# Optimization experiments

Measured on AMD Instinct MI355X. Metric: run time of the kernel, lower is better.

The kernel has to match this reference:

```python
import jax, jax.numpy as jnp
import numpy as np

DIM, DEPTH, HEADS, DIM_HEAD, MLP = 768, 6, 12, 64, 3072
INNER = HEADS * DIM_HEAD
B, N = 8, 1024
SCALE = DIM_HEAD ** -0.5
EPS = 1e-5


def _ln(x, g, b):
    m = jnp.mean(x, -1, keepdims=True)
    v = jnp.mean(jnp.square(x - m), -1, keepdims=True)
    return (x - m) * jax.lax.rsqrt(v + EPS) * g + b


def _ternary(w):
    # BitNet-style ternary quant with straight-through estimator
    s = jnp.mean(jnp.abs(w)) + 1e-8
    wq = jnp.clip(jnp.round(w / s), -1.0, 1.0) * s
    return w + jax.lax.stop_gradient(wq - w)


def setup_inputs() -> dict:
    key = jax.random.key(0)
    ks = jax.random.split(key, 8)
    d = {
        'x': jax.random.normal(ks[0], (B, N, DIM), jnp.float32),
        'ln1_g': jnp.ones((DEPTH, DIM), jnp.float32),
        'ln1_b': jnp.zeros((DEPTH, DIM), jnp.float32),
        'Wqkv': jax.random.normal(ks[1], (DEPTH, 3 * INNER, DIM), jnp.float32) * 0.02,
        'ln2_g': jnp.ones((DEPTH, INNER), jnp.float32),
        'ln2_b': jnp.zeros((DEPTH, INNER), jnp.float32),
        'Wo': jax.random.normal(ks[2], (DEPTH, DIM, INNER), jnp.float32) * 0.02,
        'bo': jnp.zeros((DEPTH, DIM), jnp.float32),
        'ffln1_g': jnp.ones((DEPTH, DIM), jnp.float32),
        'ffln1_b': jnp.zeros((DEPTH, DIM), jnp.float32),
        'W1': jax.random.normal(ks[3], (DEPTH, MLP, DIM), jnp.float32) * 0.02,
        'b1': jnp.zeros((DEPTH, MLP), jnp.float32),
        'ffln2_g': jnp.ones((DEPTH, MLP), jnp.float32),
        'ffln2_b': jnp.zeros((DEPTH, MLP), jnp.float32),
        'W2': jax.random.normal(ks[4], (DEPTH, DIM, MLP), jnp.float32) * 0.02,
        'b2': jnp.zeros((DEPTH, DIM), jnp.float32),
    }
    return d


def _forward(x, ln1_g, ln1_b, Wqkv, ln2_g, ln2_b, Wo, bo,
             ffln1_g, ffln1_b, W1, b1, ffln2_g, ffln2_b, W2, b2):
    depth = Wqkv.shape[0]
    # layers 0..depth-2 ternary, last layer plain linear
    flag = jnp.concatenate([jnp.ones((depth - 1,), x.dtype), jnp.zeros((1,), x.dtype)])

    def block(h, p):
        (g1, b1n, wqkv, g2, b2n, wo, bo_, fg1, fb1, w1, bb1, fg2, fb2, w2, bb2, f) = p

        def mt(w):
            return f * _ternary(w) + (1.0 - f) * w

        y = _ln(h, g1, b1n)
        qkv = jnp.einsum('bnd,ed->bne', y, mt(wqkv))  # [B,N,3*INNER]
        q, k, v = jnp.split(qkv, 3, axis=-1)
        def heads(t):
            return t.reshape(B, N, HEADS, DIM_HEAD).transpose(0, 2, 1, 3)
        q, k, v = heads(q), heads(k), heads(v)
        attn = jax.nn.softmax(jnp.einsum('bhnd,bhmd->bhnm', q, k) * SCALE, axis=-1)
        o = jnp.einsum('bhnm,bhmd->bhnd', attn, v)
        o = o.transpose(0, 2, 1, 3).reshape(B, N, INNER)
        o = _ln(o, g2, b2n)
        o = jnp.einsum('bne,de->bnd', o, mt(wo)) + bo_
        h = h + o
        y = _ln(h, fg1, fb1)
        y = jnp.einsum('bnd,md->bnm', y, mt(w1)) + bb1
        y = jax.nn.gelu(y, approximate=False)
        y = _ln(y, fg2, fb2)
        y = jnp.einsum('bnm,dm->bnd', y, mt(w2)) + bb2
        return h + y, None

    xs = (ln1_g, ln1_b, Wqkv, ln2_g, ln2_b, Wo, bo,
          ffln1_g, ffln1_b, W1, b1, ffln2_g, ffln2_b, W2, b2, flag)
    out, _ = jax.lax.scan(block, x, xs)
    return out


def reference(x, ln1_g, ln1_b, Wqkv, ln2_g, ln2_b, Wo, bo,
              ffln1_g, ffln1_b, W1, b1, ffln2_g, ffln2_b, W2, b2):
    return _forward(x, ln1_g, ln1_b, Wqkv, ln2_g, ln2_b, Wo, bo,
                    ffln1_g, ffln1_b, W1, b1, ffln2_g, ffln2_b, W2, b2)
```

## Files before the change

### kernel.cpp

```cpp
#include <hip/hip_runtime.h>
#include <hip/hip_bf16.h>
#include <math.h>

typedef __bf16 bf16_t;
typedef __bf16 bf16x4 __attribute__((ext_vector_type(4)));
typedef __bf16 bf16x8 __attribute__((ext_vector_type(8)));
typedef float  f32x4  __attribute__((ext_vector_type(4)));

#define TOKENS 8192
#define DIMV   768
#define INNERV 768
#define QKVW   2304
#define MLPW   3072
#define NSEQ   1024
#define NB     8
#define NH     12
#define DH     64

enum { EP_STORE = 0, EP_BIAS_RES = 1, EP_BIAS_GELU = 2 };

__device__ __forceinline__ void gload_lds16(const bf16_t* g, bf16_t* l)
{
  __builtin_amdgcn_global_load_lds((const __attribute__((address_space(1))) void*)g,
                                   (__attribute__((address_space(3))) void*)l,
                                   16, 0, 0);
}

__global__ __launch_bounds__(256)
void gemm_nt(const bf16_t* __restrict__ A, const bf16_t* __restrict__ B,
             const int K, const int N, const int mode,
             const float* __restrict__ sacc_p, const float sinvn, const float sbias,
             const float* __restrict__ bias,
             float* __restrict__ resid,
             bf16_t* __restrict__ outb,
             float* __restrict__ fout)
{
  __shared__ __align__(16) bf16_t lsA[2][128 * 32];
  __shared__ __align__(16) bf16_t lsB[2][128 * 32];
  const int tid  = threadIdx.x;
  const int lane = tid & 63;
  const int wave = tid >> 6;
  const int wm = wave >> 1, wn = wave & 1;
  const int bm = blockIdx.x, bn = blockIdx.y;

  const int srow = wave * 32 + (lane >> 2);
  const int fsw  = (srow >> 1) & 3;
  const int scol = ((lane & 3) ^ fsw) * 8;
  const bf16_t* gA = A + (size_t)(bm * 128 + srow) * K + scol;
  const bf16_t* gB = B + (size_t)(bn * 128 + srow) * K + scol;
  const int l0 = srow * 32 + (lane & 3) * 8;
  const int l1 = (srow + 16) * 32 + (lane & 3) * 8;

  f32x4 acc[4][4];
#pragma unroll
  for (int i = 0; i < 4; i++)
#pragma unroll
    for (int j = 0; j < 4; j++) acc[i][j] = (f32x4){0.f, 0.f, 0.f, 0.f};

  const int fr   = ((lane & 15) >> 1) & 3;
  const int rsl  = ((lane >> 4) ^ fr) * 8;
  const int arow = (wm * 64 + (lane & 15)) * 32 + rsl;
  const int brow = (wn * 64 + (lane & 15)) * 32 + rsl;

  auto stage = [&](int b, int kb) {
    gload_lds16(gA + kb,                  &lsA[b][l0]);
    gload_lds16(gA + (size_t)16 * K + kb, &lsA[b][l1]);
    gload_lds16(gB + kb,                  &lsB[b][l0]);
    gload_lds16(gB + (size_t)16 * K + kb, &lsB[b][l1]);
  };
  auto compute = [&](int b) {
    bf16x8 af[4], bfv[4];
#pragma unroll
    for (int i = 0; i < 4; i++) af[i]  = *(const bf16x8*)&lsA[b][arow + i * 16 * 32];
#pragma unroll
    for (int j = 0; j < 4; j++) bfv[j] = *(const bf16x8*)&lsB[b][brow + j * 16 * 32];
#pragma unroll
    for (int i = 0; i < 4; i++)
#pragma unroll
      for (int j = 0; j < 4; j++)
        acc[i][j] = __builtin_amdgcn_mfma_f32_16x16x32_bf16(af[i], bfv[j], acc[i][j], 0, 0, 0);
  };

  const int NT = K / 32;
  stage(0, 0);
  stage(1, 32);
  int cur = 0;
  for (int t = 0; t < NT - 1; ++t) {
    asm volatile("s_waitcnt vmcnt(4)" ::: "memory");
    __builtin_amdgcn_s_barrier();
    __builtin_amdgcn_sched_barrier(0);
    compute(cur);
    asm volatile("s_waitcnt lgkmcnt(0)" ::: "memory");
    __builtin_amdgcn_s_barrier();
    __builtin_amdgcn_sched_barrier(0);
    if (t + 2 < NT) stage(cur, (t + 2) * 32);
    cur ^= 1;
  }
  asm volatile("s_waitcnt vmcnt(0)" ::: "memory");
  __builtin_amdgcn_s_barrier();
  __builtin_amdgcn_sched_barrier(0);
  compute(cur);

  const float s = (*sacc_p) * sinvn + sbias;
  const int r0 = bm * 128 + wm * 64 + (lane >> 4) * 4;
  const int c0 = bn * 128 + wn * 64 + (lane & 15);
#pragma unroll
  for (int i = 0; i < 4; i++) {
#pragma unroll
    for (int j = 0; j < 4; j++) {
      const int col = c0 + j * 16;
#pragma unroll
      for (int r = 0; r < 4; r++) {
        const int row = r0 + i * 16 + r;
        const float v = acc[i][j][r] * s;
        const size_t idx = (size_t)row * N + col;
        if (mode == EP_STORE) {
          outb[idx] = (bf16_t)v;
        } else if (mode == EP_BIAS_RES) {
          const float add = v + bias[col];
          if (fout) fout[idx] = resid[idx] + add;
          else      resid[idx] += add;
        } else {
          const float t = v + bias[col];
          outb[idx] = (bf16_t)(0.5f * t * (1.0f + erff(t * 0.70710678118654752f)));
        }
      }
    }
  }
}

template <typename TIN>
__global__ __launch_bounds__(256)
void ln_kern(const TIN* __restrict__ x, const float* __restrict__ g,
             const float* __restrict__ b, bf16_t* __restrict__ y, const int W)
{
  const int row = blockIdx.x;
  const int tid = threadIdx.x;
  const TIN* xr = x + (size_t)row * W;
  float s = 0.f, s2 = 0.f;
  if constexpr (sizeof(TIN) == 4) {
    const f32x4* xv = (const f32x4*)xr;
    for (int i = tid; i < W / 4; i += 256) {
      f32x4 v = xv[i];
#pragma unroll
      for (int e = 0; e < 4; e++) { s += v[e]; s2 += v[e] * v[e]; }
    }
  } else {
    const bf16x8* xv = (const bf16x8*)xr;
    for (int i = tid; i < W / 8; i += 256) {
      bf16x8 v = xv[i];
#pragma unroll
      for (int e = 0; e < 8; e++) { const float f = (float)v[e]; s += f; s2 += f * f; }
    }
  }
#pragma unroll
  for (int off = 32; off > 0; off >>= 1) {
    s  += __shfl_xor(s,  off, 64);
    s2 += __shfl_xor(s2, off, 64);
  }
  __shared__ float red[8];
  if ((tid & 63) == 0) { red[(tid >> 6) * 2] = s; red[(tid >> 6) * 2 + 1] = s2; }
  __syncthreads();
  const float ts  = red[0] + red[2] + red[4] + red[6];
  const float ts2 = red[1] + red[3] + red[5] + red[7];
  const float invW = 1.0f / (float)W;
  const float mean = ts * invW;
  const float var  = fmaxf(ts2 * invW - mean * mean, 0.f);
  const float rs   = rsqrtf(var + 1e-5f);
  bf16_t* yr = y + (size_t)row * W;
  const f32x4* gv = (const f32x4*)g;
  const f32x4* bv = (const f32x4*)b;
  if constexpr (sizeof(TIN) == 4) {
    const f32x4* xv = (const f32x4*)xr;
    bf16x4* yv = (bf16x4*)yr;
    for (int i = tid; i < W / 4; i += 256) {
      f32x4 v = xv[i], gg = gv[i], bb = bv[i];
      bf16x4 o;
#pragma unroll
      for (int e = 0; e < 4; e++) o[e] = (bf16_t)((v[e] - mean) * rs * gg[e] + bb[e]);
      yv[i] = o;
    }
  } else {
    const bf16x8* xv = (const bf16x8*)xr;
    bf16x8* yv = (bf16x8*)yr;
    for (int i = tid; i < W / 8; i += 256) {
      bf16x8 v = xv[i];
      f32x4 g0 = gv[2 * i], g1 = gv[2 * i + 1];
      f32x4 b0 = bv[2 * i], b1 = bv[2 * i + 1];
      bf16x8 o;
#pragma unroll
      for (int e = 0; e < 4; e++) o[e]     = (bf16_t)(((float)v[e]     - mean) * rs * g0[e] + b0[e]);
#pragma unroll
      for (int e = 0; e < 4; e++) o[e + 4] = (bf16_t)(((float)v[e + 4] - mean) * rs * g1[e] + b1[e]);
      yv[i] = o;
    }
  }
}

__global__ __launch_bounds__(256)
void attn_mfma(const bf16_t* __restrict__ qkv, bf16_t* __restrict__ o)
{
  __shared__ __align__(16) bf16_t Ks[64][72];
  __shared__ __align__(16) bf16_t Vt[64][72];
  __shared__ __align__(16) bf16_t Pw[4][16][72];
  const float SCL = 0.125f * 1.44269504088896f;
  const int tid  = threadIdx.x;
  const int lane = tid & 63;
  const int wave = tid >> 6;
  const int quad = lane >> 4;
  const int l15  = lane & 15;
  const int qb = blockIdx.x, hh = blockIdx.y, bb = blockIdx.z;
  const size_t tokbase = (size_t)bb * NSEQ;

  const int qrow = qb * 64 + wave * 16 + l15;
  bf16x8 qf[2];
  {
    const bf16_t* qp = qkv + (tokbase + qrow) * QKVW + hh * DH;
    qf[0] = *(const bf16x8*)(qp + quad * 8);
    qf[1] = *(const bf16x8*)(qp + 32 + quad * 8);
  }

  f32x4 Ot[4];
#pragma unroll
  for (int i = 0; i < 4; i++) Ot[i] = (f32x4){0.f, 0.f, 0.f, 0.f};
  float m2[4], lp[4];
#pragma unroll
  for (int r = 0; r < 4; r++) { m2[r] = -1e30f; lp[r] = 0.f; }

  const int skv = tid & 63;
  const int sd  = (tid >> 6) * 16;

  bf16x8 k0, k1, v0, v1;
  {
    const bf16_t* kp = qkv + (tokbase + skv) * QKVW + INNERV + hh * DH + sd;
    k0 = *(const bf16x8*)kp;
    k1 = *(const bf16x8*)(kp + 8);
    v0 = *(const bf16x8*)(kp + INNERV);
    v1 = *(const bf16x8*)(kp + INNERV + 8);
  }

  for (int kt = 0; kt < NSEQ / 64; ++kt) {
    __syncthreads();
    *(bf16x8*)&Ks[skv][sd]     = k0;
    *(bf16x8*)&Ks[skv][sd + 8] = k1;
#pragma unroll
    for (int e = 0; e < 8; e++) { Vt[sd + e][skv] = v0[e]; Vt[sd + 8 + e][skv] = v1[e]; }
    __syncthreads();

    bf16x8 nk0 = k0, nk1 = k1, nv0 = v0, nv1 = v1;
    if (kt + 1 < NSEQ / 64) {
      const bf16_t* kp = qkv + (tokbase + (kt + 1) * 64 + skv) * QKVW + INNERV + hh * DH + sd;
      nk0 = *(const bf16x8*)kp;
      nk1 = *(const bf16x8*)(kp + 8);
      nv0 = *(const bf16x8*)(kp + INNERV);
      nv1 = *(const bf16x8*)(kp + INNERV + 8);
    }

    f32x4 st[4];
    __builtin_amdgcn_s_setprio(1);
#pragma unroll
    for (int nt = 0; nt < 4; nt++) {
      bf16x8 b0 = *(const bf16x8*)&Ks[nt * 16 + l15][quad * 8];
      bf16x8 b1 = *(const bf16x8*)&Ks[nt * 16 + l15][32 + quad * 8];
      f32x4 c = (f32x4){0.f, 0.f, 0.f, 0.f};
      c = __builtin_amdgcn_mfma_f32_16x16x32_bf16(qf[0], b0, c, 0, 0, 0);
      c = __builtin_amdgcn_mfma_f32_16x16x32_bf16(qf[1], b1, c, 0, 0, 0);
      st[nt] = c;
    }
    __builtin_amdgcn_s_setprio(0);

    float rmax2[4];
#pragma unroll
    for (int r = 0; r < 4; r++) {
      float v = fmaxf(fmaxf(st[0][r], st[1][r]), fmaxf(st[2][r], st[3][r]));
      v = fmaxf(v, __shfl_xor(v, 1, 64));
      v = fmaxf(v, __shfl_xor(v, 2, 64));
      v = fmaxf(v, __shfl_xor(v, 4, 64));
      v = fmaxf(v, __shfl_xor(v, 8, 64));
      rmax2[r] = v * SCL;
    }
    const bool ok = (rmax2[0] <= m2[0] + 8.f) && (rmax2[1] <= m2[1] + 8.f) &&
                    (rmax2[2] <= m2[2] + 8.f) && (rmax2[3] <= m2[3] + 8.f);
    if (!__all(ok)) {
#pragma unroll
      for (int r = 0; r < 4; r++) {
        const float mnew = fmaxf(m2[r], rmax2[r]);
        const float alpha = exp2f(m2[r] - mnew);
        m2[r] = mnew;
        lp[r] *= alpha;
#pragma unroll
        for (int dt = 0; dt < 4; dt++) Ot[dt][r] *= alpha;
      }
    }
#pragma unroll
    for (int nt = 0; nt < 4; nt++) {
#pragma unroll
      for (int r = 0; r < 4; r++) {
        const float p = exp2f(fmaf(st[nt][r], SCL, -m2[r]));
        lp[r] += p;
        Pw[wave][quad * 4 + r][nt * 16 + l15] = (bf16_t)p;
      }
    }

    asm volatile("s_waitcnt lgkmcnt(0)" ::: "memory");
    __builtin_amdgcn_sched_barrier(0);

    __builtin_amdgcn_s_setprio(1);
#pragma unroll
    for (int kk = 0; kk < 2; kk++) {
      bf16x8 pa = *(const bf16x8*)&Pw[wave][l15][kk * 32 + quad * 8];
#pragma unroll
      for (int dt = 0; dt < 4; dt++) {
        bf16x8 vb = *(const bf16x8*)&Vt[dt * 16 + l15][kk * 32 + quad * 8];
        Ot[dt] = __builtin_amdgcn_mfma_f32_16x16x32_bf16(pa, vb, Ot[dt], 0, 0, 0);
      }
    }
    __builtin_amdgcn_s_setprio(0);

    k0 = nk0; k1 = nk1; v0 = nv0; v1 = nv1;
  }

  float inv[4];
#pragma unroll
  for (int r = 0; r < 4; r++) {
    float v = lp[r];
    v += __shfl_xor(v, 1, 64);
    v += __shfl_xor(v, 2, 64);
    v += __shfl_xor(v, 4, 64);
    v += __shfl_xor(v, 8, 64);
    inv[r] = 1.0f / v;
  }
#pragma unroll
  for (int dt = 0; dt < 4; dt++) {
#pragma unroll
    for (int r = 0; r < 4; r++) {
      const int q = qb * 64 + wave * 16 + quad * 4 + r;
      const int d = dt * 16 + l15;
      o[(tokbase + q) * INNERV + hh * DH + d] = (bf16_t)(Ot[dt][r] * inv[r]);
    }
  }
}

__global__ __launch_bounds__(64)
void zero_kern(float* __restrict__ p)
{
  p[threadIdx.x] = 0.f;
}

__global__ __launch_bounds__(256)
void absmean4_kern(const float* __restrict__ w0, const float* __restrict__ w1,
                   const float* __restrict__ w2, const float* __restrict__ w3,
                   const long n0, const long n1, const long n2, const long n3,
                   float* __restrict__ acc)
{
  const int t = blockIdx.y;
  const float* w = (t == 0) ? w0 : (t == 1) ? w1 : (t == 2) ? w2 : w3;
  const long  n  = (t == 0) ? n0 : (t == 1) ? n1 : (t == 2) ? n2 : n3;
  const int tid = threadIdx.x;
  float s = 0.f;
  const size_t stride = (size_t)256 * gridDim.x * 4;
  for (size_t i = ((size_t)blockIdx.x * 256 + tid) * 4; i < (size_t)n; i += stride) {
    f32x4 v = *(const f32x4*)(w + i);
    s += fabsf(v[0]) + fabsf(v[1]) + fabsf(v[2]) + fabsf(v[3]);
  }
#pragma unroll
  for (int off = 32; off > 0; off >>= 1) s += __shfl_xor(s, off, 64);
  __shared__ float red[4];
  if ((tid & 63) == 0) red[tid >> 6] = s;
  __syncthreads();
  if (tid == 0) atomicAdd(&acc[t], red[0] + red[1] + red[2] + red[3]);
}

__global__ __launch_bounds__(256)
void quant4_kern(const float* __restrict__ w0, const float* __restrict__ w1,
                 const float* __restrict__ w2, const float* __restrict__ w3,
                 bf16_t* __restrict__ q0, bf16_t* __restrict__ q1,
                 bf16_t* __restrict__ q2, bf16_t* __restrict__ q3,
                 const int n40, const int n41, const int n42, const int n43,
                 const float* __restrict__ acc,
                 const float inv0, const float inv1, const float inv2, const float inv3)
{
  const int t = blockIdx.y;
  const float* w = (t == 0) ? w0 : (t == 1) ? w1 : (t == 2) ? w2 : w3;
  bf16_t*      q = (t == 0) ? q0 : (t == 1) ? q1 : (t == 2) ? q2 : q3;
  const int   n4 = (t == 0) ? n40 : (t == 1) ? n41 : (t == 2) ? n42 : n43;
  const float iv = (t == 0) ? inv0 : (t == 1) ? inv1 : (t == 2) ? inv2 : inv3;
  const int i = blockIdx.x * 256 + threadIdx.x;
  if (i >= n4) return;
  const float s = acc[t] * iv + 1e-8f;
  f32x4 v = ((const f32x4*)w)[i];
  bf16x4 o;
#pragma unroll
  for (int e = 0; e < 4; e++) {
    float qv = rintf(v[e] / s);
    qv = fminf(1.f, fmaxf(-1.f, qv));
    o[e] = (bf16_t)qv;
  }
  ((bf16x4*)q)[i] = o;
}

__global__ __launch_bounds__(256)
void cast4_kern(const float* __restrict__ w0, const float* __restrict__ w1,
                const float* __restrict__ w2, const float* __restrict__ w3,
                bf16_t* __restrict__ q0, bf16_t* __restrict__ q1,
                bf16_t* __restrict__ q2, bf16_t* __restrict__ q3,
                const int n40, const int n41, const int n42, const int n43)
{
  const int t = blockIdx.y;
  const float* w = (t == 0) ? w0 : (t == 1) ? w1 : (t == 2) ? w2 : w3;
  bf16_t*      q = (t == 0) ? q0 : (t == 1) ? q1 : (t == 2) ? q2 : q3;
  const int   n4 = (t == 0) ? n40 : (t == 1) ? n41 : (t == 2) ? n42 : n43;
  const int i = blockIdx.x * 256 + threadIdx.x;
  if (i >= n4) return;
  f32x4 v = ((const f32x4*)w)[i];
  bf16x4 o;
#pragma unroll
  for (int e = 0; e < 4; e++) o[e] = (bf16_t)v[e];
  ((bf16x4*)q)[i] = o;
}

__global__ __launch_bounds__(256)
void copyf_kern(const float* __restrict__ in, float* __restrict__ out, const int n4)
{
  const int i = blockIdx.x * 256 + threadIdx.x;
  if (i < n4) ((f32x4*)out)[i] = ((const f32x4*)in)[i];
}

extern "C" void kernel_launch(void* const* d_in, const int* in_sizes, int n_in,
                              void* d_out, int out_size, void* d_ws, size_t ws_size,
                              hipStream_t stream)
{
  const float* x     = (const float*)d_in[0];
  const float* ln1_g = (const float*)d_in[1];
  const float* ln1_b = (const float*)d_in[2];
  const float* Wqkv  = (const float*)d_in[3];
  const float* ln2_g = (const float*)d_in[4];
  const float* ln2_b = (const float*)d_in[5];
  const float* Wo    = (const float*)d_in[6];
  const float* bo    = (const float*)d_in[7];
  const float* fg1   = (const float*)d_in[8];
  const float* fb1   = (const float*)d_in[9];
  const float* W1    = (const float*)d_in[10];
  const float* b1    = (const float*)d_in[11];
  const float* fg2   = (const float*)d_in[12];
  const float* fb2   = (const float*)d_in[13];
  const float* W2    = (const float*)d_in[14];
  const float* b2    = (const float*)d_in[15];

  char* ws = (char*)d_ws;
  size_t off = 0;
  float*  sacc  = (float*)(ws + off);  off += 256;
  float*  h     = (float*)(ws + off);  off += (size_t)TOKENS * DIMV * 4;
  bf16_t* bigA  = (bf16_t*)(ws + off); off += (size_t)TOKENS * MLPW * 2;
  bf16_t* bigB  = (bf16_t*)(ws + off); off += (size_t)TOKENS * MLPW * 2;
  bf16_t* q_qkv = (bf16_t*)(ws + off); off += (size_t)QKVW * DIMV * 2;
  bf16_t* q_o   = (bf16_t*)(ws + off); off += (size_t)DIMV * INNERV * 2;
  bf16_t* q_1   = (bf16_t*)(ws + off); off += (size_t)MLPW * DIMV * 2;
  bf16_t* q_2   = (bf16_t*)(ws + off); off += (size_t)DIMV * MLPW * 2;

  bf16_t* obuf   = bigA;
  bf16_t* ln2out = bigA + (size_t)TOKENS * INNERV;

  zero_kern<<<1, 64, 0, stream>>>(sacc);
  copyf_kern<<<TOKENS * DIMV / 4 / 256, 256, 0, stream>>>(x, h, TOKENS * DIMV / 4);

  for (int lyr = 0; lyr < 6; ++lyr) {
    const float* wqkv_l = Wqkv + (size_t)lyr * QKVW * DIMV;
    const float* wo_l   = Wo   + (size_t)lyr * DIMV * INNERV;
    const float* w1_l   = W1   + (size_t)lyr * MLPW * DIMV;
    const float* w2_l   = W2   + (size_t)lyr * DIMV * MLPW;
    const float *sq, *so, *s1, *s2p;
    float iq, io, i1, i2, bq, bo2, bb1v, bb2v;
    if (lyr < 5) {
      absmean4_kern<<<dim3(64, 4), 256, 0, stream>>>(
          wqkv_l, wo_l, w1_l, w2_l,
          (long)QKVW * DIMV, (long)DIMV * INNERV, (long)MLPW * DIMV, (long)DIMV * MLPW,
          &sacc[lyr * 4]);
      quant4_kern<<<dim3(MLPW * DIMV / 1024, 4), 256, 0, stream>>>(
          wqkv_l, wo_l, w1_l, w2_l, q_qkv, q_o, q_1, q_2,
          QKVW * DIMV / 4, DIMV * INNERV / 4, MLPW * DIMV / 4, DIMV * MLPW / 4,
          &sacc[lyr * 4],
          1.0f / (QKVW * DIMV), 1.0f / (DIMV * INNERV), 1.0f / (MLPW * DIMV), 1.0f / (DIMV * MLPW));
      sq = &sacc[lyr * 4 + 0]; iq = 1.0f / (QKVW * DIMV); bq = 1e-8f;
      so = &sacc[lyr * 4 + 1]; io = 1.0f / (DIMV * INNERV); bo2 = 1e-8f;
      s1 = &sacc[lyr * 4 + 2]; i1 = 1.0f / (MLPW * DIMV); bb1v = 1e-8f;
      s2p = &sacc[lyr * 4 + 3]; i2 = 1.0f / (DIMV * MLPW); bb2v = 1e-8f;
    } else {
      cast4_kern<<<dim3(MLPW * DIMV / 1024, 4), 256, 0, stream>>>(
          wqkv_l, wo_l, w1_l, w2_l, q_qkv, q_o, q_1, q_2,
          QKVW * DIMV / 4, DIMV * INNERV / 4, MLPW * DIMV / 4, DIMV * MLPW / 4);
      sq = so = s1 = s2p = &sacc[63];
      iq = io = i1 = i2 = 0.f;
      bq = bo2 = bb1v = bb2v = 1.0f;
    }

    ln_kern<float><<<TOKENS, 256, 0, stream>>>(h, ln1_g + lyr * DIMV, ln1_b + lyr * DIMV, bigA, DIMV);
    gemm_nt<<<dim3(64, QKVW / 128), 256, 0, stream>>>(bigA, q_qkv, DIMV, QKVW, EP_STORE, sq, iq, bq, nullptr, nullptr, bigB, nullptr);
    attn_mfma<<<dim3(NSEQ / 64, NH, NB), 256, 0, stream>>>(bigB, obuf);
    ln_kern<bf16_t><<<TOKENS, 256, 0, stream>>>(obuf, ln2_g + lyr * INNERV, ln2_b + lyr * INNERV, ln2out, INNERV);
    gemm_nt<<<dim3(64, DIMV / 128), 256, 0, stream>>>(ln2out, q_o, INNERV, DIMV, EP_BIAS_RES, so, io, bo2, bo + lyr * DIMV, h, nullptr, nullptr);
    ln_kern<float><<<TOKENS, 256, 0, stream>>>(h, fg1 + lyr * DIMV, fb1 + lyr * DIMV, bigA, DIMV);
    gemm_nt<<<dim3(64, MLPW / 128), 256, 0, stream>>>(bigA, q_1, DIMV, MLPW, EP_BIAS_GELU, s1, i1, bb1v, b1 + lyr * MLPW, nullptr, bigB, nullptr);
    ln_kern<bf16_t><<<TOKENS, 256, 0, stream>>>(bigB, fg2 + lyr * MLPW, fb2 + lyr * MLPW, bigA, MLPW);
    gemm_nt<<<dim3(64, DIMV / 128), 256, 0, stream>>>(bigA, q_2, MLPW, DIMV, EP_BIAS_RES, s2p, i2, bb2v, b2 + lyr * DIMV, h, nullptr,
                                                      (lyr == 5) ? (float*)d_out : nullptr);
  }
}
```

Baseline: 2.534 ms.

## Use single-wave 64x64 GEMM tiles, fast GELU, and lazy softmax max reduction

Replaces the 256-thread 128x128 GEMM with a one-wave 64x64 kernel that needs no block barriers, so there are many more blocks and no s_barrier stalls. The trade-off is half the data reuse per tile, which doubles global/LDS traffic. It also swaps erff in the GELU epilogue for an Abramowitz-Stegun polynomial approximation, which trades a small amount of accuracy for fewer instructions. In attention, the cross-lane max shuffles now run only when the rescale branch is taken; the skip check uses per-lane maxima.

```diff
diff --git a/kernel.cpp b/kernel.cpp
--- a/kernel.cpp
+++ b/kernel.cpp
@@ -26,8 +26,24 @@
                                    16, 0, 0);
 }
 
-__global__ __launch_bounds__(256)
-void gemm_nt(const bf16_t* __restrict__ A, const bf16_t* __restrict__ B,
+__device__ __forceinline__ float gelu_fast(float x)
+{
+  const float z = fabsf(x) * 0.70710678118654752f;
+  const float d = fmaf(0.3275911f, z, 1.0f);
+  const float t = 1.0f / d;
+  float p = fmaf(t, 1.061405429f, -1.453152027f);
+  p = fmaf(t, p, 1.421413741f);
+  p = fmaf(t, p, -0.284496736f);
+  p = fmaf(t, p, 0.254829592f);
+  p = t * p;
+  const float e = __expf(-z * z);
+  float erfv = fmaf(-p, e, 1.0f);
+  erfv = copysignf(erfv, x);
+  return 0.5f * x * (1.0f + erfv);
+}
+
+__global__ __launch_bounds__(64)
+void gemm_wv(const bf16_t* __restrict__ A, const bf16_t* __restrict__ B,
              const int K, const int N, const int mode,
              const float* __restrict__ sacc_p, const float sinvn, const float sbias,
              const float* __restrict__ bias,
@@ -35,21 +51,19 @@
              bf16_t* __restrict__ outb,
              float* __restrict__ fout)
 {
-  __shared__ __align__(16) bf16_t lsA[2][128 * 32];
-  __shared__ __align__(16) bf16_t lsB[2][128 * 32];
-  const int tid  = threadIdx.x;
-  const int lane = tid & 63;
-  const int wave = tid >> 6;
-  const int wm = wave >> 1, wn = wave & 1;
+  __shared__ __align__(16) bf16_t lsA[2][64 * 32];
+  __shared__ __align__(16) bf16_t lsB[2][64 * 32];
+  const int lane = threadIdx.x;
+  const int quad = lane >> 4;
+  const int l15  = lane & 15;
   const int bm = blockIdx.x, bn = blockIdx.y;
 
-  const int srow = wave * 32 + (lane >> 2);
+  const int srow = lane >> 2;
   const int fsw  = (srow >> 1) & 3;
   const int scol = ((lane & 3) ^ fsw) * 8;
-  const bf16_t* gA = A + (size_t)(bm * 128 + srow) * K + scol;
-  const bf16_t* gB = B + (size_t)(bn * 128 + srow) * K + scol;
-  const int l0 = srow * 32 + (lane & 3) * 8;
-  const int l1 = (srow + 16) * 32 + (lane & 3) * 8;
+  const bf16_t* gA = A + (size_t)(bm * 64 + srow) * K + scol;
+  const bf16_t* gB = B + (size_t)(bn * 64 + srow) * K + scol;
+  const int ldst = srow * 32 + (lane & 3) * 8;
 
   f32x4 acc[4][4];
 #pragma unroll
@@ -57,23 +71,23 @@
 #pragma unroll
     for (int j = 0; j < 4; j++) acc[i][j] = (f32x4){0.f, 0.f, 0.f, 0.f};
 
-  const int fr   = ((lane & 15) >> 1) & 3;
-  const int rsl  = ((lane >> 4) ^ fr) * 8;
-  const int arow = (wm * 64 + (lane & 15)) * 32 + rsl;
-  const int brow = (wn * 64 + (lane & 15)) * 32 + rsl;
+  const int fr  = (l15 >> 1) & 3;
+  const int rsl = (quad ^ fr) * 8;
+  const int frow = l15 * 32 + rsl;
 
   auto stage = [&](int b, int kb) {
-    gload_lds16(gA + kb,                  &lsA[b][l0]);
-    gload_lds16(gA + (size_t)16 * K + kb, &lsA[b][l1]);
-    gload_lds16(gB + kb,                  &lsB[b][l0]);
-    gload_lds16(gB + (size_t)16 * K + kb, &lsB[b][l1]);
+#pragma unroll
+    for (int j = 0; j < 4; j++) {
+      gload_lds16(gA + (size_t)j * 16 * K + kb, &lsA[b][ldst + j * 16 * 32]);
+      gload_lds16(gB + (size_t)j * 16 * K + kb, &lsB[b][ldst + j * 16 * 32]);
+    }
   };
   auto compute = [&](int b) {
     bf16x8 af[4], bfv[4];
 #pragma unroll
-    for (int i = 0; i < 4; i++) af[i]  = *(const bf16x8*)&lsA[b][arow + i * 16 * 32];
-#pragma unroll
-    for (int j = 0; j < 4; j++) bfv[j] = *(const bf16x8*)&lsB[b][brow + j * 16 * 32];
+    for (int i = 0; i < 4; i++) af[i]  = *(const bf16x8*)&lsA[b][frow + i * 16 * 32];
+#pragma unroll
+    for (int j = 0; j < 4; j++) bfv[j] = *(const bf16x8*)&lsB[b][frow + j * 16 * 32];
 #pragma unroll
     for (int i = 0; i < 4; i++)
 #pragma unroll
@@ -86,24 +100,21 @@
   stage(1, 32);
   int cur = 0;
   for (int t = 0; t < NT - 1; ++t) {
-    asm volatile("s_waitcnt vmcnt(4)" ::: "memory");
-    __builtin_amdgcn_s_barrier();
+    asm volatile("s_waitcnt vmcnt(8)" ::: "memory");
     __builtin_amdgcn_sched_barrier(0);
     compute(cur);
     asm volatile("s_waitcnt lgkmcnt(0)" ::: "memory");
-    __builtin_amdgcn_s_barrier();
     __builtin_amdgcn_sched_barrier(0);
     if (t + 2 < NT) stage(cur, (t + 2) * 32);
     cur ^= 1;
   }
   asm volatile("s_waitcnt vmcnt(0)" ::: "memory");
-  __builtin_amdgcn_s_barrier();
   __builtin_amdgcn_sched_barrier(0);
   compute(cur);
 
   const float s = (*sacc_p) * sinvn + sbias;
-  const int r0 = bm * 128 + wm * 64 + (lane >> 4) * 4;
-  const int c0 = bn * 128 + wn * 64 + (lane & 15);
+  const int r0 = bm * 64 + quad * 4;
+  const int c0 = bn * 64 + l15;
 #pragma unroll
   for (int i = 0; i < 4; i++) {
 #pragma unroll
@@ -121,8 +132,7 @@
           if (fout) fout[idx] = resid[idx] + add;
           else      resid[idx] += add;
         } else {
-          const float t = v + bias[col];
-          outb[idx] = (bf16_t)(0.5f * t * (1.0f + erff(t * 0.70710678118654752f)));
+          outb[idx] = (bf16_t)gelu_fast(v + bias[col]);
         }
       }
     }
@@ -269,22 +279,22 @@
     }
     __builtin_amdgcn_s_setprio(0);
 
-    float rmax2[4];
-#pragma unroll
-    for (int r = 0; r < 4; r++) {
-      float v = fmaxf(fmaxf(st[0][r], st[1][r]), fmaxf(st[2][r], st[3][r]));
-      v = fmaxf(v, __shfl_xor(v, 1, 64));
-      v = fmaxf(v, __shfl_xor(v, 2, 64));
-      v = fmaxf(v, __shfl_xor(v, 4, 64));
-      v = fmaxf(v, __shfl_xor(v, 8, 64));
-      rmax2[r] = v * SCL;
-    }
-    const bool ok = (rmax2[0] <= m2[0] + 8.f) && (rmax2[1] <= m2[1] + 8.f) &&
-                    (rmax2[2] <= m2[2] + 8.f) && (rmax2[3] <= m2[3] + 8.f);
+    float lm[4];
+#pragma unroll
+    for (int r = 0; r < 4; r++)
+      lm[r] = fmaxf(fmaxf(st[0][r], st[1][r]), fmaxf(st[2][r], st[3][r]));
+    const bool ok = (lm[0] * SCL <= m2[0] + 8.f) && (lm[1] * SCL <= m2[1] + 8.f) &&
+                    (lm[2] * SCL <= m2[2] + 8.f) && (lm[3] * SCL <= m2[3] + 8.f);
     if (!__all(ok)) {
 #pragma unroll
       for (int r = 0; r < 4; r++) {
-        const float mnew = fmaxf(m2[r], rmax2[r]);
+        float v = lm[r];
+        v = fmaxf(v, __shfl_xor(v, 1, 64));
+        v = fmaxf(v, __shfl_xor(v, 2, 64));
+        v = fmaxf(v, __shfl_xor(v, 4, 64));
+        v = fmaxf(v, __shfl_xor(v, 8, 64));
+        const float rmax2 = v * SCL;
+        const float mnew = fmaxf(m2[r], rmax2);
         const float alpha = exp2f(m2[r] - mnew);
         m2[r] = mnew;
         lp[r] *= alpha;
@@ -495,14 +505,14 @@
     }
 
     ln_kern<float><<<TOKENS, 256, 0, stream>>>(h, ln1_g + lyr * DIMV, ln1_b + lyr * DIMV, bigA, DIMV);
-    gemm_nt<<<dim3(64, QKVW / 128), 256, 0, stream>>>(bigA, q_qkv, DIMV, QKVW, EP_STORE, sq, iq, bq, nullptr, nullptr, bigB, nullptr);
+    gemm_wv<<<dim3(TOKENS / 64, QKVW / 64), 64, 0, stream>>>(bigA, q_qkv, DIMV, QKVW, EP_STORE, sq, iq, bq, nullptr, nullptr, bigB, nullptr);
     attn_mfma<<<dim3(NSEQ / 64, NH, NB), 256, 0, stream>>>(bigB, obuf);
     ln_kern<bf16_t><<<TOKENS, 256, 0, stream>>>(obuf, ln2_g + lyr * INNERV, ln2_b + lyr * INNERV, ln2out, INNERV);
-    gemm_nt<<<dim3(64, DIMV / 128), 256, 0, stream>>>(ln2out, q_o, INNERV, DIMV, EP_BIAS_RES, so, io, bo2, bo + lyr * DIMV, h, nullptr, nullptr);
+    gemm_wv<<<dim3(TOKENS / 64, DIMV / 64), 64, 0, stream>>>(ln2out, q_o, INNERV, DIMV, EP_BIAS_RES, so, io, bo2, bo + lyr * DIMV, h, nullptr, nullptr);
     ln_kern<float><<<TOKENS, 256, 0, stream>>>(h, fg1 + lyr * DIMV, fb1 + lyr * DIMV, bigA, DIMV);
-    gemm_nt<<<dim3(64, MLPW / 128), 256, 0, stream>>>(bigA, q_1, DIMV, MLPW, EP_BIAS_GELU, s1, i1, bb1v, b1 + lyr * MLPW, nullptr, bigB, nullptr);
+    gemm_wv<<<dim3(TOKENS / 64, MLPW / 64), 64, 0, stream>>>(bigA, q_1, DIMV, MLPW, EP_BIAS_GELU, s1, i1, bb1v, b1 + lyr * MLPW, nullptr, bigB, nullptr);
     ln_kern<bf16_t><<<TOKENS, 256, 0, stream>>>(bigB, fg2 + lyr * MLPW, fb2 + lyr * MLPW, bigA, MLPW);
-    gemm_nt<<<dim3(64, DIMV / 128), 256, 0, stream>>>(bigA, q_2, MLPW, DIMV, EP_BIAS_RES, s2p, i2, bb2v, b2 + lyr * DIMV, h, nullptr,
-                                                      (lyr == 5) ? (float*)d_out : nullptr);
-  }
-}
+    gemm_wv<<<dim3(TOKENS / 64, DIMV / 64), 64, 0, stream>>>(bigA, q_2, MLPW, DIMV, EP_BIAS_RES, s2p, i2, bb2v, b2 + lyr * DIMV, h, nullptr,
+                                                             (lyr == 5) ? (float*)d_out : nullptr);
+  }
+}
```

Result: slower. 2.852 ms (+12.5%).
